# Optimization experiments

Hardware: AMD Instinct MI355X
Metric: run time of the kernel (lower is better)

## Reference

```python
import jax, jax.numpy as jnp
import numpy as np

N = 20000      # nodes
E = 320000     # edges
F = 128        # feat_dim
N_RBF = 20
CUTOFF = 5.0


def setup_inputs() -> dict:
    key = jax.random.key(0)
    ks = jax.random.split(key, 12)
    h_i = jax.random.normal(ks[0], (N, F), dtype=jnp.float32)
    v_i = jax.random.normal(ks[1], (N, F, 3), dtype=jnp.float32)
    # distances in (0, cutoff); keep strictly > 0 to avoid div-by-zero in sinc basis
    d_ij = (jax.random.uniform(ks[2], (E,), dtype=jnp.float32) * 0.98 + 0.01) * CUTOFF
    r = jax.random.normal(ks[3], (E, 3), dtype=jnp.float32)
    unit_r_ij = r / jnp.linalg.norm(r, axis=-1, keepdims=True)
    nbrs = jax.random.randint(ks[4], (E, 2), 0, N, dtype=jnp.int64)
    # params: layers = Dense(F->F, swish) then Dense(F->3F); dist_embed dense: n_rbf -> 3F
    s1 = 1.0 / np.sqrt(F)
    W1 = jax.random.uniform(ks[5], (F, F), jnp.float32, -s1, s1)
    b1 = jax.random.uniform(ks[6], (F,), jnp.float32, -s1, s1)
    W2 = jax.random.uniform(ks[7], (F, 3 * F), jnp.float32, -s1, s1)
    b2 = jax.random.uniform(ks[8], (3 * F,), jnp.float32, -s1, s1)
    sr = 1.0 / np.sqrt(N_RBF)
    Wr = jax.random.uniform(ks[9], (N_RBF, 3 * F), jnp.float32, -sr, sr)
    br = jax.random.uniform(ks[10], (3 * F,), jnp.float32, -sr, sr)
    return {"h_i": h_i, "v_i": v_i, "d_ij": d_ij, "unit_r_ij": unit_r_ij,
            "nbrs": nbrs, "W1": W1, "b1": b1, "W2": W2, "b2": b2, "Wr": Wr, "br": br}


def _dist_embed(d, Wr, br):
    # PaiNN sinc-like radial basis: sin(n*pi*d/cutoff)/d, n=1..N_RBF
    n = jnp.arange(1, N_RBF + 1, dtype=d.dtype)
    rbf = jnp.sin(n[None, :] * jnp.pi * d[:, None] / CUTOFF) / d[:, None]  # [E, N_RBF]
    # cosine cutoff envelope
    fcut = 0.5 * (jnp.cos(jnp.pi * d / CUTOFF) + 1.0) * (d < CUTOFF)       # [E]
    return (rbf @ Wr + br) * fcut[:, None]                                  # [E, 3F]


def reference(h_i, v_i, d_ij, unit_r_ij, nbrs, W1, b1, W2, b2, Wr, br):
    # phi = Dense(swish) -> Dense : [N, 3F]
    phi = jax.nn.silu(h_i @ W1 + b1) @ W2 + b2
    src = nbrs[:, 1]
    dst = nbrs[:, 0]
    edge_inv = phi[src] * _dist_embed(d_ij, Wr, br)          # [E, 3F]
    edge_inv = edge_inv.reshape(edge_inv.shape[0], 3, F)     # [E, 3, F]
    f1, f2, f3 = edge_inv[:, 0], edge_inv[:, 1], edge_inv[:, 2]
    # dv: [E, F, 3]
    dv = f1[:, :, None] * unit_r_ij[:, None, :] + f2[:, :, None] * v_i[src]
    dh_i = jax.ops.segment_sum(f3, dst, num_segments=N)      # [N, F]
    dv_i = jax.ops.segment_sum(dv, dst, num_segments=N)      # [N, F, 3]
    return (dh_i, dv_i)
```

## Files before the change

kernel.cpp:

```cpp
#include <hip/hip_runtime.h>
#include <math.h>

#define F 128
#define THREEF 384
#define N_RBF 20
#define CUTOFF 5.0f
#define CAP 64

__global__ __launch_bounds__(256) void mlp_kernel(
    const float* __restrict__ h, const float* __restrict__ W1,
    const float* __restrict__ b1, const float* __restrict__ W2,
    const float* __restrict__ b2, float* __restrict__ phi, int N)
{
    __shared__ float sh_h[16 * F];
    __shared__ float sh_t[16 * F];
    const int tid   = threadIdx.x;
    const int node0 = blockIdx.x * 16;

    {
        const float4* src = (const float4*)(h + (size_t)node0 * F);
        float4* dst = (float4*)sh_h;
        dst[tid]       = src[tid];
        dst[tid + 256] = src[tid + 256];
    }
    __syncthreads();

    const int j2 = tid & 63;
    const int r0 = (tid >> 6) * 4;

    {
        float acc[4][2];
        const float bb0 = b1[j2], bb1 = b1[j2 + 64];
        #pragma unroll
        for (int r = 0; r < 4; ++r) { acc[r][0] = bb0; acc[r][1] = bb1; }
        for (int k4 = 0; k4 < F; k4 += 4) {
            float4 a[4];
            #pragma unroll
            for (int r = 0; r < 4; ++r)
                a[r] = *(const float4*)&sh_h[(r0 + r) * F + k4];
            #pragma unroll
            for (int kk = 0; kk < 4; ++kk) {
                const float w0  = W1[(k4 + kk) * F + j2];
                const float w1v = W1[(k4 + kk) * F + j2 + 64];
                #pragma unroll
                for (int r = 0; r < 4; ++r) {
                    const float av = ((const float*)&a[r])[kk];
                    acc[r][0] = fmaf(av, w0,  acc[r][0]);
                    acc[r][1] = fmaf(av, w1v, acc[r][1]);
                }
            }
        }
        #pragma unroll
        for (int r = 0; r < 4; ++r) {
            const float x0 = acc[r][0], x1 = acc[r][1];
            sh_t[(r0 + r) * F + j2]      = x0 / (1.0f + __expf(-x0));
            sh_t[(r0 + r) * F + j2 + 64] = x1 / (1.0f + __expf(-x1));
        }
    }
    __syncthreads();

    {
        float acc[4][6];
        #pragma unroll
        for (int c = 0; c < 6; ++c) {
            const float bb = b2[j2 + c * 64];
            #pragma unroll
            for (int r = 0; r < 4; ++r) acc[r][c] = bb;
        }
        for (int k4 = 0; k4 < F; k4 += 4) {
            float4 a[4];
            #pragma unroll
            for (int r = 0; r < 4; ++r)
                a[r] = *(const float4*)&sh_t[(r0 + r) * F + k4];
            #pragma unroll
            for (int kk = 0; kk < 4; ++kk) {
                float w[6];
                #pragma unroll
                for (int c = 0; c < 6; ++c)
                    w[c] = W2[(k4 + kk) * THREEF + j2 + c * 64];
                #pragma unroll
                for (int r = 0; r < 4; ++r) {
                    const float av = ((const float*)&a[r])[kk];
                    #pragma unroll
                    for (int c = 0; c < 6; ++c)
                        acc[r][c] = fmaf(av, w[c], acc[r][c]);
                }
            }
        }
        #pragma unroll
        for (int r = 0; r < 4; ++r) {
            #pragma unroll
            for (int c = 0; c < 6; ++c) {
                const int col = j2 + c * 64;
                const int p   = col >> 7;
                const int fc  = col & 127;
                phi[(size_t)p * N * F + (size_t)(node0 + r0 + r) * F + fc] = acc[r][c];
            }
        }
    }
}

__global__ __launch_bounds__(256) void wrt_kernel(
    const float* __restrict__ Wr, float* __restrict__ WrT)
{
    const int idx = blockIdx.x * 256 + threadIdx.x;
    if (idx >= 5 * 3 * 128) return;
    const int f  = idx & 127;
    const int c  = (idx >> 7) % 3;
    const int n4 = idx / (3 * 128);
    float4 v;
    v.x = Wr[(4 * n4 + 0) * THREEF + c * 128 + f];
    v.y = Wr[(4 * n4 + 1) * THREEF + c * 128 + f];
    v.z = Wr[(4 * n4 + 2) * THREEF + c * 128 + f];
    v.w = Wr[(4 * n4 + 3) * THREEF + c * 128 + f];
    ((float4*)WrT)[idx] = v;
}

__global__ __launch_bounds__(256) void build_kernel(
    const float* __restrict__ d_ij, const float* __restrict__ unit_r,
    const int* __restrict__ nbrs, int* __restrict__ cnt,
    int* __restrict__ eid, float* __restrict__ pack, int E)
{
    int e = blockIdx.x * 256 + threadIdx.x;
    if (e >= E) return;
    const int2 nb = ((const int2*)nbrs)[e];
    const int dst = nb.x;
    const int src = nb.y;
    const int slot = atomicAdd(&cnt[dst], 1);
    if (slot < CAP) eid[dst * CAP + slot] = e;

    const float d = d_ij[e];
    const float x = (float)M_PI * d * (1.0f / CUTOFF);
    float sx, cx;
    __sincosf(x, &sx, &cx);
    const float fcut = (d < CUTOFF) ? 0.5f * (cx + 1.0f) : 0.0f;
    float4 q0, q1;
    q0.x = sx * fcut / d;
    q0.y = 2.0f * cx;
    q0.z = fcut;
    q0.w = unit_r[3 * e + 0];
    q1.x = unit_r[3 * e + 1];
    q1.y = unit_r[3 * e + 2];
    q1.z = __int_as_float(src);
    q1.w = 0.0f;
    float4* pk = (float4*)(pack + (size_t)e * 8);
    pk[0] = q0;
    pk[1] = q1;
}

__global__ __launch_bounds__(128) void gather_kernel(
    const float* __restrict__ phi,
    const float* __restrict__ v_i,
    const float* __restrict__ WrT,
    const float* __restrict__ br,
    const int*   __restrict__ cnt,
    const int*   __restrict__ eid,
    const float* __restrict__ pack,
    float* __restrict__ dh,
    float* __restrict__ dv,
    int N)
{
    const int node = blockIdx.x;
    const int f    = threadIdx.x;

    const float br0 = br[f], br1 = br[f + 128], br2 = br[f + 256];

    const int deg0 = cnt[node];
    const int deg  = deg0 < CAP ? deg0 : CAP;
    const int* my_eid = eid + node * CAP;

    const float* phi0 = phi;
    const float* phi1 = phi + (size_t)N * F;
    const float* phi2 = phi + (size_t)2 * N * F;
    const float4* wT  = (const float4*)WrT;

    float dh_acc = 0.0f, dv0 = 0.0f, dv1 = 0.0f, dv2 = 0.0f;

    for (int i = 0; i < deg; ++i) {
        const int e = __builtin_amdgcn_readfirstlane(my_eid[i]);
        const float* pk = pack + (size_t)e * 8;
        const float s1   = pk[0];
        const float twoc = pk[1];
        const float fcut = pk[2];
        const float ux   = pk[3];
        const float uy   = pk[4];
        const float uz   = pk[5];
        const int src = __builtin_amdgcn_readfirstlane(__float_as_int(pk[6]));

        float a0 = br0 * fcut, a1 = br1 * fcut, a2 = br2 * fcut;
        float rp = 0.0f, rc = s1;
        #pragma unroll
        for (int n4 = 0; n4 < 5; ++n4) {
            const float4 w0 = wT[(n4 * 3 + 0) * 128 + f];
            const float4 w1 = wT[(n4 * 3 + 1) * 128 + f];
            const float4 w2 = wT[(n4 * 3 + 2) * 128 + f];
            #pragma unroll
            for (int k = 0; k < 4; ++k) {
                const float wa = ((const float*)&w0)[k];
                const float wb = ((const float*)&w1)[k];
                const float wc = ((const float*)&w2)[k];
                a0 = fmaf(rc, wa, a0);
                a1 = fmaf(rc, wb, a1);
                a2 = fmaf(rc, wc, a2);
                const float rn = fmaf(twoc, rc, -rp);
                rp = rc;
                rc = rn;
            }
        }

        const float f1 = phi0[(size_t)src * F + f] * a0;
        const float f2 = phi1[(size_t)src * F + f] * a1;
        const float f3 = phi2[(size_t)src * F + f] * a2;

        dh_acc += f3;

        const float* vs = v_i + (size_t)src * THREEF + 3 * f;
        dv0 = fmaf(f1, ux, fmaf(f2, vs[0], dv0));
        dv1 = fmaf(f1, uy, fmaf(f2, vs[1], dv1));
        dv2 = fmaf(f1, uz, fmaf(f2, vs[2], dv2));
    }

    dh[(size_t)node * F + f] = dh_acc;
    float* dvp = dv + (size_t)node * THREEF + 3 * f;
    dvp[0] = dv0;
    dvp[1] = dv1;
    dvp[2] = dv2;
}

extern "C" void kernel_launch(void* const* d_in, const int* in_sizes, int n_in,
                              void* d_out, int out_size, void* d_ws, size_t ws_size,
                              hipStream_t stream) {
    const float* h_i    = (const float*)d_in[0];
    const float* v_i    = (const float*)d_in[1];
    const float* d_ij   = (const float*)d_in[2];
    const float* unit_r = (const float*)d_in[3];
    const int*   nbrs   = (const int*)  d_in[4];
    const float* W1     = (const float*)d_in[5];
    const float* b1     = (const float*)d_in[6];
    const float* W2     = (const float*)d_in[7];
    const float* b2     = (const float*)d_in[8];
    const float* Wr     = (const float*)d_in[9];
    const float* br     = (const float*)d_in[10];

    const int N = in_sizes[0] / F;
    const int E = in_sizes[2];

    float* dh = (float*)d_out;
    float* dv = dh + (size_t)N * F;

    float* phi  = (float*)d_ws;
    float* pack = phi + (size_t)3 * N * F;
    float* WrT  = pack + (size_t)E * 8;
    int*   cnt  = (int*)(WrT + 5 * 3 * 128 * 4);
    int*   eid  = cnt + N;

    hipMemsetAsync(cnt, 0, (size_t)N * sizeof(int), stream);

    mlp_kernel<<<(N + 15) / 16, 256, 0, stream>>>(h_i, W1, b1, W2, b2, phi, N);
    wrt_kernel<<<8, 256, 0, stream>>>(Wr, WrT);
    build_kernel<<<(E + 255) / 256, 256, 0, stream>>>(d_ij, unit_r, nbrs, cnt,
                                                      eid, pack, E);
    gather_kernel<<<N, 128, 0, stream>>>(phi, v_i, WrT, br, cnt, eid, pack,
                                         dh, dv, N);
}
```

Before: 310.8 us.

## Run node MLP on bf16 MFMA matrix cores with pre-transposed weights

Replaces the scalar-FMA fp32 node MLP with a kernel that casts h to bf16 and uses 16x16x32 bf16 MFMA instructions for both dense layers, staging the swish output through padded LDS per wave. A new small kernel transposes and casts W1 and W2 to bf16 each call. This targets the compute cost of the MLP stage but lowers precision of phi to bf16 inputs, which may affect accuracy tolerance.

```diff
diff --git a/kernel.cpp b/kernel.cpp
--- a/kernel.cpp
+++ b/kernel.cpp
@@ -6,96 +6,99 @@
 #define N_RBF 20
 #define CUTOFF 5.0f
 #define CAP 64
-
-__global__ __launch_bounds__(256) void mlp_kernel(
-    const float* __restrict__ h, const float* __restrict__ W1,
-    const float* __restrict__ b1, const float* __restrict__ W2,
-    const float* __restrict__ b2, float* __restrict__ phi, int N)
-{
-    __shared__ float sh_h[16 * F];
-    __shared__ float sh_t[16 * F];
-    const int tid   = threadIdx.x;
-    const int node0 = blockIdx.x * 16;
-
-    {
-        const float4* src = (const float4*)(h + (size_t)node0 * F);
-        float4* dst = (float4*)sh_h;
-        dst[tid]       = src[tid];
-        dst[tid + 256] = src[tid + 256];
-    }
-    __syncthreads();
-
-    const int j2 = tid & 63;
-    const int r0 = (tid >> 6) * 4;
-
-    {
-        float acc[4][2];
-        const float bb0 = b1[j2], bb1 = b1[j2 + 64];
-        #pragma unroll
-        for (int r = 0; r < 4; ++r) { acc[r][0] = bb0; acc[r][1] = bb1; }
-        for (int k4 = 0; k4 < F; k4 += 4) {
-            float4 a[4];
-            #pragma unroll
-            for (int r = 0; r < 4; ++r)
-                a[r] = *(const float4*)&sh_h[(r0 + r) * F + k4];
-            #pragma unroll
-            for (int kk = 0; kk < 4; ++kk) {
-                const float w0  = W1[(k4 + kk) * F + j2];
-                const float w1v = W1[(k4 + kk) * F + j2 + 64];
-                #pragma unroll
-                for (int r = 0; r < 4; ++r) {
-                    const float av = ((const float*)&a[r])[kk];
-                    acc[r][0] = fmaf(av, w0,  acc[r][0]);
-                    acc[r][1] = fmaf(av, w1v, acc[r][1]);
-                }
-            }
-        }
-        #pragma unroll
-        for (int r = 0; r < 4; ++r) {
-            const float x0 = acc[r][0], x1 = acc[r][1];
-            sh_t[(r0 + r) * F + j2]      = x0 / (1.0f + __expf(-x0));
-            sh_t[(r0 + r) * F + j2 + 64] = x1 / (1.0f + __expf(-x1));
-        }
-    }
-    __syncthreads();
-
-    {
-        float acc[4][6];
-        #pragma unroll
-        for (int c = 0; c < 6; ++c) {
-            const float bb = b2[j2 + c * 64];
-            #pragma unroll
-            for (int r = 0; r < 4; ++r) acc[r][c] = bb;
-        }
-        for (int k4 = 0; k4 < F; k4 += 4) {
-            float4 a[4];
-            #pragma unroll
-            for (int r = 0; r < 4; ++r)
-                a[r] = *(const float4*)&sh_t[(r0 + r) * F + k4];
-            #pragma unroll
-            for (int kk = 0; kk < 4; ++kk) {
-                float w[6];
-                #pragma unroll
-                for (int c = 0; c < 6; ++c)
-                    w[c] = W2[(k4 + kk) * THREEF + j2 + c * 64];
-                #pragma unroll
-                for (int r = 0; r < 4; ++r) {
-                    const float av = ((const float*)&a[r])[kk];
-                    #pragma unroll
-                    for (int c = 0; c < 6; ++c)
-                        acc[r][c] = fmaf(av, w[c], acc[r][c]);
-                }
-            }
-        }
-        #pragma unroll
-        for (int r = 0; r < 4; ++r) {
-            #pragma unroll
-            for (int c = 0; c < 6; ++c) {
-                const int col = j2 + c * 64;
-                const int p   = col >> 7;
-                const int fc  = col & 127;
-                phi[(size_t)p * N * F + (size_t)(node0 + r0 + r) * F + fc] = acc[r][c];
-            }
+#define TLDS_STRIDE 136
+
+typedef __bf16 bf16x8 __attribute__((ext_vector_type(8)));
+typedef float  f32x4  __attribute__((ext_vector_type(4)));
+
+__global__ __launch_bounds__(256) void wcast_kernel(
+    const float* __restrict__ W1, const float* __restrict__ W2,
+    __bf16* __restrict__ W1T, __bf16* __restrict__ W2T)
+{
+    const int idx = blockIdx.x * 256 + threadIdx.x;
+    if (idx < 128 * 128) {
+        const int n = idx >> 7, k = idx & 127;
+        W1T[idx] = (__bf16)W1[k * F + n];
+    }
+    if (idx < 384 * 128) {
+        const int n = idx >> 7, k = idx & 127;
+        W2T[idx] = (__bf16)W2[k * THREEF + n];
+    }
+}
+
+__global__ __launch_bounds__(256) void mlp_mfma_kernel(
+    const float* __restrict__ h,
+    const __bf16* __restrict__ W1T,
+    const float* __restrict__ b1,
+    const __bf16* __restrict__ W2T,
+    const float* __restrict__ b2,
+    float* __restrict__ phi, int N)
+{
+    __shared__ __bf16 t_lds[4][16 * TLDS_STRIDE];
+
+    const int wave = threadIdx.x >> 6;
+    const int lane = threadIdx.x & 63;
+    const int m    = lane & 15;
+    const int quad = lane >> 4;
+    const int node0 = blockIdx.x * 64 + wave * 16;
+    if (node0 >= N) return;
+
+    bf16x8 a1[4];
+    #pragma unroll
+    for (int kb = 0; kb < 4; ++kb) {
+        const float* hp = h + (size_t)(node0 + m) * F + kb * 32 + quad * 8;
+        const float4 x0 = *(const float4*)hp;
+        const float4 x1 = *(const float4*)(hp + 4);
+        bf16x8 a;
+        a[0] = (__bf16)x0.x; a[1] = (__bf16)x0.y;
+        a[2] = (__bf16)x0.z; a[3] = (__bf16)x0.w;
+        a[4] = (__bf16)x1.x; a[5] = (__bf16)x1.y;
+        a[6] = (__bf16)x1.z; a[7] = (__bf16)x1.w;
+        a1[kb] = a;
+    }
+
+    #pragma unroll
+    for (int ct = 0; ct < 8; ++ct) {
+        f32x4 acc = {0.0f, 0.0f, 0.0f, 0.0f};
+        #pragma unroll
+        for (int kb = 0; kb < 4; ++kb) {
+            const bf16x8 b =
+                *(const bf16x8*)(W1T + (size_t)(ct * 16 + m) * F + kb * 32 + quad * 8);
+            acc = __builtin_amdgcn_mfma_f32_16x16x32_bf16(a1[kb], b, acc, 0, 0, 0);
+        }
+        const int col = ct * 16 + m;
+        const float bb = b1[col];
+        #pragma unroll
+        for (int reg = 0; reg < 4; ++reg) {
+            const float x = acc[reg] + bb;
+            const float s = x / (1.0f + __expf(-x));
+            t_lds[wave][(quad * 4 + reg) * TLDS_STRIDE + col] = (__bf16)s;
+        }
+    }
+
+    bf16x8 a2[4];
+    #pragma unroll
+    for (int kb = 0; kb < 4; ++kb)
+        a2[kb] = *(const bf16x8*)&t_lds[wave][m * TLDS_STRIDE + kb * 32 + quad * 8];
+
+    #pragma unroll
+    for (int ct = 0; ct < 24; ++ct) {
+        f32x4 acc = {0.0f, 0.0f, 0.0f, 0.0f};
+        #pragma unroll
+        for (int kb = 0; kb < 4; ++kb) {
+            const bf16x8 b =
+                *(const bf16x8*)(W2T + (size_t)(ct * 16 + m) * F + kb * 32 + quad * 8);
+            acc = __builtin_amdgcn_mfma_f32_16x16x32_bf16(a2[kb], b, acc, 0, 0, 0);
+        }
+        const int col   = ct * 16 + m;
+        const int plane = col >> 7;
+        const int fc    = col & 127;
+        const float bb  = b2[col];
+        float* pp = phi + (size_t)plane * N * F + fc;
+        #pragma unroll
+        for (int reg = 0; reg < 4; ++reg) {
+            const int row = quad * 4 + reg;
+            pp[(size_t)(node0 + row) * F] = acc[reg] + bb;
         }
     }
 }
@@ -248,15 +251,19 @@
     float* dh = (float*)d_out;
     float* dv = dh + (size_t)N * F;
 
-    float* phi  = (float*)d_ws;
-    float* pack = phi + (size_t)3 * N * F;
-    float* WrT  = pack + (size_t)E * 8;
-    int*   cnt  = (int*)(WrT + 5 * 3 * 128 * 4);
-    int*   eid  = cnt + N;
+    float*  phi  = (float*)d_ws;
+    float*  pack = phi + (size_t)3 * N * F;
+    float*  WrT  = pack + (size_t)E * 8;
+    int*    cnt  = (int*)(WrT + 5 * 3 * 128 * 4);
+    int*    eid  = cnt + N;
+    __bf16* W1T  = (__bf16*)(eid + (size_t)N * CAP);
+    __bf16* W2T  = W1T + 128 * 128;
 
     hipMemsetAsync(cnt, 0, (size_t)N * sizeof(int), stream);
 
-    mlp_kernel<<<(N + 15) / 16, 256, 0, stream>>>(h_i, W1, b1, W2, b2, phi, N);
+    wcast_kernel<<<192, 256, 0, stream>>>(W1, W2, W1T, W2T);
+    mlp_mfma_kernel<<<(N + 63) / 64, 256, 0, stream>>>(h_i, W1T, b1, W2T, b2,
+                                                       phi, N);
     wrt_kernel<<<8, 256, 0, stream>>>(Wr, WrT);
     build_kernel<<<(E + 255) / 256, 256, 0, stream>>>(d_ij, unit_r, nbrs, cnt,
                                                       eid, pack, E);
```

Result: faster. 299.3 us (-3.7%).
